# Optimization experiments

Hardware: AMD Instinct MI355X
Metric: run time of the kernel (lower is better)

## Reference

```python
import jax, jax.numpy as jnp
import numpy as np

B, S, D, CH = 1024, 64, 256, 1024


def setup_inputs() -> dict:
    key = jax.random.key(0)
    ks = jax.random.split(key, 8)
    sc = 0.05
    return {
        "local_descs_t": jax.random.normal(ks[0], (B, S, D), jnp.float32),
        "local_descs_rot": jax.random.normal(ks[1], (B, S, D), jnp.float32),
        "W_scene": jax.random.normal(ks[2], (2 * D, 1), jnp.float32) * sc,
        "b_scene": jnp.zeros((1,), jnp.float32),
        "Wt_h": jax.random.normal(ks[3], (S, D, CH), jnp.float32) * sc,
        "bt_h": jnp.zeros((S, CH), jnp.float32),
        "Wt_o": jax.random.normal(ks[4], (S, CH, 3), jnp.float32) * sc,
        "bt_o": jnp.zeros((S, 3), jnp.float32),
        "Wr_h": jax.random.normal(ks[5], (S, D, CH), jnp.float32) * sc,
        "br_h": jnp.zeros((S, CH), jnp.float32),
        "Wr_o": jax.random.normal(ks[6], (S, CH, 4), jnp.float32) * sc,
        "br_o": jnp.zeros((S, 4), jnp.float32),
    }


def reference(local_descs_t, local_descs_rot, W_scene, b_scene,
              Wt_h, bt_h, Wt_o, bt_o, Wr_h, br_h, Wr_o, br_o):
    # scene classifier: Linear(2D -> 1) on concat descriptors, log-softmax over scenes
    cat = jnp.concatenate((local_descs_t, local_descs_rot), axis=2)  # [B,S,2D]
    logits = jnp.einsum('bsd,do->bso', cat, W_scene)[..., 0] + b_scene[0]  # [B,S]
    scene_log_distr = jax.nn.log_softmax(logits, axis=1)
    max_idx = jnp.argmax(scene_log_distr, axis=1)  # [B] top-1 scene per sample

    b = jnp.arange(local_descs_t.shape[0])
    g_t = local_descs_t[b, max_idx]      # [B,D] one-hot gather of selected scene
    g_rot = local_descs_rot[b, max_idx]  # [B,D]

    h_t = jax.nn.gelu(jnp.einsum('bd,bdh->bh', g_t, Wt_h[max_idx]) + bt_h[max_idx],
                      approximate=False)
    x_t = jnp.einsum('bh,bho->bo', h_t, Wt_o[max_idx]) + bt_o[max_idx]  # [B,3]
    h_r = jax.nn.gelu(jnp.einsum('bd,bdh->bh', g_rot, Wr_h[max_idx]) + br_h[max_idx],
                      approximate=False)
    x_rot = jnp.einsum('bh,bho->bo', h_r, Wr_o[max_idx]) + br_o[max_idx]  # [B,4]

    expected_pose = jnp.concatenate((x_t, x_rot), axis=1)  # [B,7]
    return expected_pose, scene_log_distr
```

## Files before the change

kernel.cpp:

```cpp
#include <hip/hip_runtime.h>
#include <math.h>

#define BN 1024
#define SN 64
#define DN 256
#define CHN 1024
#define GRP 16

__device__ __forceinline__ float gelu_exact(float x) {
    return 0.5f * x * (1.0f + erff(x * 0.70710678118654752440f));
}

__global__ __launch_bounds__(256, 4) void k_scene(
    const float* __restrict__ dt, const float* __restrict__ dr,
    const float* __restrict__ Wsc, const float* __restrict__ bsc,
    const float* __restrict__ bt_o, const float* __restrict__ br_o,
    float* __restrict__ out_logd, float* __restrict__ pose,
    int* __restrict__ counts, int* __restrict__ lists)
{
    int b = blockIdx.x;
    int tid = threadIdx.x;
    int lane = tid & 63;
    int wave = tid >> 6;
    __shared__ float part[SN][65];
    __shared__ float logits[SN];

    float4 wt = *(const float4*)&Wsc[4 * lane];
    float4 wr = *(const float4*)&Wsc[DN + 4 * lane];
    const float* pt = dt + (size_t)b * SN * DN + 4 * lane;
    const float* pr = dr + (size_t)b * SN * DN + 4 * lane;
    float bias0 = bsc[0];

    float p[16];
    #pragma unroll 8
    for (int k = 0; k < 16; k++) {
        int s = wave * 16 + k;
        float4 t4 = *(const float4*)&pt[s * DN];
        float4 r4 = *(const float4*)&pr[s * DN];
        p[k] = t4.x * wt.x + t4.y * wt.y + t4.z * wt.z + t4.w * wt.w
             + r4.x * wr.x + r4.y * wr.y + r4.z * wr.z + r4.w * wr.w;
    }
    #pragma unroll
    for (int k = 0; k < 16; k++) part[wave * 16 + k][lane] = p[k];
    __syncthreads();

    {
        int s = tid >> 2, q = tid & 3;
        float sum = 0.f;
        #pragma unroll
        for (int j = 0; j < 16; j++) sum += part[s][q * 16 + j];
        sum += __shfl_xor(sum, 1);
        sum += __shfl_xor(sum, 2);
        if (q == 0) logits[s] = sum + bias0;
    }
    __syncthreads();

    if (wave == 0) {
        float l = logits[lane];
        float m = l; int idx = lane;
        #pragma unroll
        for (int off = 32; off >= 1; off >>= 1) {
            float om = __shfl_xor(m, off);
            int oidx = __shfl_xor(idx, off);
            if (om > m || (om == m && oidx < idx)) { m = om; idx = oidx; }
        }
        float e = expf(l - m);
        float ssum = e;
        #pragma unroll
        for (int off = 32; off >= 1; off >>= 1) ssum += __shfl_xor(ssum, off);
        float logZ = m + logf(ssum);
        out_logd[b * SN + lane] = l - logZ;
        if (lane == 0) {
            int pos = atomicAdd(&counts[idx], 1);
            lists[idx * BN + pos] = b;
        }
        if (lane < 7)
            pose[b * 7 + lane] = (lane < 3) ? bt_o[idx * 3 + lane]
                                            : br_o[idx * 4 + (lane - 3)];
    }
}

__global__ __launch_bounds__(256, 4) void k_expert(
    const float* __restrict__ dt, const float* __restrict__ dr,
    const float* __restrict__ Wt_h, const float* __restrict__ bt_h, const float* __restrict__ Wt_o,
    const float* __restrict__ Wr_h, const float* __restrict__ br_h, const float* __restrict__ Wr_o,
    const int* __restrict__ counts, const int* __restrict__ lists,
    float* __restrict__ pose)
{
    __shared__ float g[GRP][DN];
    __shared__ int pref[SN + 1];
    __shared__ int bl[GRP];
    int tid = threadIdx.x;
    int lane = tid & 63;
    int wave = tid >> 6;

    if (wave == 0) {
        int c = counts[lane];
        int ng = (c + 15) >> 4;
        #pragma unroll
        for (int off = 1; off < 64; off <<= 1) {
            int v = __shfl_up(ng, off);
            if (lane >= off) ng += v;
        }
        pref[lane + 1] = ng;
        if (lane == 0) pref[0] = 0;
    }
    __syncthreads();

    int q = blockIdx.x;
    if (q >= pref[SN] * 8) return;

    int s = 0;
    while (pref[s + 1] * 8 <= q) s++;
    int r = q - pref[s] * 8;
    int grp = r >> 3;
    int z = (r >> 2) & 1;
    int c4 = r & 3;

    int cnt = counts[s];
    int base = grp * GRP;
    int n = min(GRP, cnt - base);

    const float* Wh; const float* bh; const float* Wo; const float* descs; int no, ob;
    if (z == 0) {
        Wh = Wt_h + (size_t)s * DN * CHN; bh = bt_h + s * CHN;
        Wo = Wt_o + (size_t)s * CHN * 3;  descs = dt; no = 3; ob = 0;
    } else {
        Wh = Wr_h + (size_t)s * DN * CHN; bh = br_h + s * CHN;
        Wo = Wr_o + (size_t)s * CHN * 4;  descs = dr; no = 4; ob = 3;
    }

    #pragma unroll 4
    for (int i = 0; i < GRP; i++) {
        int bi = 0; float v = 0.f;
        if (i < n) {
            bi = lists[s * BN + base + i];
            v = descs[(size_t)bi * SN * DN + s * DN + tid];
        }
        g[i][tid] = v;
        if (tid == 0) bl[i] = bi;
    }
    __syncthreads();

    int h0 = c4 * 256 + tid;
    const float* wp = Wh + h0;
    float acc[GRP];
    #pragma unroll
    for (int i = 0; i < GRP; i++) acc[i] = 0.f;

    for (int db = 0; db < DN; db += 8) {
        float w[8];
        #pragma unroll
        for (int rr = 0; rr < 8; rr++) w[rr] = wp[(size_t)(db + rr) * CHN];
        #pragma unroll
        for (int i = 0; i < GRP; i++) {
            float4 ga = *(const float4*)&g[i][db];
            float4 gb = *(const float4*)&g[i][db + 4];
            acc[i] += ga.x * w[0] + ga.y * w[1] + ga.z * w[2] + ga.w * w[3]
                    + gb.x * w[4] + gb.y * w[5] + gb.z * w[6] + gb.w * w[7];
        }
    }

    float hb = bh[h0];
    float wo[4];
    #pragma unroll
    for (int o = 0; o < 4; o++) wo[o] = (o < no) ? Wo[h0 * no + o] : 0.f;

    #pragma unroll
    for (int i = 0; i < GRP; i++) {
        if (i < n) {
            float hv = gelu_exact(acc[i] + hb);
            #pragma unroll
            for (int o = 0; o < 4; o++) {
                if (o < no) {
                    float p = hv * wo[o];
                    #pragma unroll
                    for (int off = 32; off >= 1; off >>= 1) p += __shfl_down(p, off);
                    if (lane == 0) atomicAdd(&pose[bl[i] * 7 + ob + o], p);
                }
            }
        }
    }
}

extern "C" void kernel_launch(void* const* d_in, const int* in_sizes, int n_in,
                              void* d_out, int out_size, void* d_ws, size_t ws_size,
                              hipStream_t stream) {
    const float* dt    = (const float*)d_in[0];
    const float* dr    = (const float*)d_in[1];
    const float* Wsc   = (const float*)d_in[2];
    const float* bsc   = (const float*)d_in[3];
    const float* Wt_h  = (const float*)d_in[4];
    const float* bt_h  = (const float*)d_in[5];
    const float* Wt_o  = (const float*)d_in[6];
    const float* bt_o  = (const float*)d_in[7];
    const float* Wr_h  = (const float*)d_in[8];
    const float* br_h  = (const float*)d_in[9];
    const float* Wr_o  = (const float*)d_in[10];
    const float* br_o  = (const float*)d_in[11];

    float* pose = (float*)d_out;
    float* logd = (float*)d_out + BN * 7;

    int* counts  = (int*)((char*)d_ws + 4096);
    int* lists   = (int*)((char*)d_ws + 8192);

    hipMemsetAsync(counts, 0, SN * sizeof(int), stream);

    k_scene<<<BN, 256, 0, stream>>>(dt, dr, Wsc, bsc, bt_o, br_o,
                                    logd, pose, counts, lists);
    k_expert<<<1024, 256, 0, stream>>>(
        dt, dr, Wt_h, bt_h, Wt_o, Wr_h, br_h, Wr_o, counts, lists, pose);
}
```

Measured before the change: 303.3 us.

## Double expert group size, split reduction dim across half-blocks, double-buffer weight loads

Expert groups grow from 16 to 32 samples, so each expert hidden-weight column is streamed from memory half as often per sample. To keep per-thread work bounded, each block covers 128 hidden columns and splits the D reduction between its two 128-thread halves, combining partial sums through shared memory. Weight loads are double-buffered to overlap with the FMAs, and descriptor gathers use float4. The cost is more accumulator registers, an extra shared-memory combine with barriers, and idle upper-half threads during the GELU and output epilogue.

```diff
diff --git a/kernel.cpp b/kernel.cpp
--- a/kernel.cpp
+++ b/kernel.cpp
@@ -5,7 +5,7 @@
 #define SN 64
 #define DN 256
 #define CHN 1024
-#define GRP 16
+#define GRP 32
 
 __device__ __forceinline__ float gelu_exact(float x) {
     return 0.5f * x * (1.0f + erff(x * 0.70710678118654752440f));
@@ -92,11 +92,11 @@
     __shared__ int bl[GRP];
     int tid = threadIdx.x;
     int lane = tid & 63;
-    int wave = tid >> 6;
-
-    if (wave == 0) {
+    int wavei = tid >> 6;
+
+    if (wavei == 0) {
         int c = counts[lane];
-        int ng = (c + 15) >> 4;
+        int ng = (c + GRP - 1) >> 5;
         #pragma unroll
         for (int off = 1; off < 64; off <<= 1) {
             int v = __shfl_up(ng, off);
@@ -108,18 +108,22 @@
     __syncthreads();
 
     int q = blockIdx.x;
-    if (q >= pref[SN] * 8) return;
+    if (q >= pref[SN] * 16) return;
 
     int s = 0;
-    while (pref[s + 1] * 8 <= q) s++;
-    int r = q - pref[s] * 8;
-    int grp = r >> 3;
-    int z = (r >> 2) & 1;
-    int c4 = r & 3;
+    while (pref[s + 1] * 16 <= q) s++;
+    int r = q - pref[s] * 16;
+    int grp = r >> 4;
+    int z = (r >> 3) & 1;
+    int chunk = r & 7;
 
     int cnt = counts[s];
     int base = grp * GRP;
     int n = min(GRP, cnt - base);
+
+    int col = tid & 127;
+    int dh = tid >> 7;
+    int h0 = (chunk << 7) + col;
 
     const float* Wh; const float* bh; const float* Wo; const float* descs; int no, ob;
     if (z == 0) {
@@ -130,36 +134,64 @@
         Wo = Wr_o + (size_t)s * CHN * 4;  descs = dr; no = 4; ob = 3;
     }
 
-    #pragma unroll 4
-    for (int i = 0; i < GRP; i++) {
-        int bi = 0; float v = 0.f;
+    #pragma unroll 2
+    for (int ii = 0; ii < 8; ii++) {
+        int i = ii * 4 + wavei;
+        int bi = 0;
+        float4 v = make_float4(0.f, 0.f, 0.f, 0.f);
         if (i < n) {
             bi = lists[s * BN + base + i];
-            v = descs[(size_t)bi * SN * DN + s * DN + tid];
-        }
-        g[i][tid] = v;
-        if (tid == 0) bl[i] = bi;
-    }
-    __syncthreads();
-
-    int h0 = c4 * 256 + tid;
-    const float* wp = Wh + h0;
+            v = *(const float4*)&descs[(size_t)bi * SN * DN + s * DN + 4 * lane];
+        }
+        *(float4*)&g[i][4 * lane] = v;
+        if (lane == 0) bl[i] = bi;
+    }
+    __syncthreads();
+
+    int d0 = dh << 7;
+    const float* wp = Wh + (size_t)d0 * CHN + h0;
+
     float acc[GRP];
     #pragma unroll
     for (int i = 0; i < GRP; i++) acc[i] = 0.f;
 
-    for (int db = 0; db < DN; db += 8) {
-        float w[8];
-        #pragma unroll
-        for (int rr = 0; rr < 8; rr++) w[rr] = wp[(size_t)(db + rr) * CHN];
+    float wa[8], wb[8];
+    #pragma unroll
+    for (int rr = 0; rr < 8; rr++) wa[rr] = wp[(size_t)rr * CHN];
+
+    auto compute = [&](const float (&w)[8], int db) {
         #pragma unroll
         for (int i = 0; i < GRP; i++) {
-            float4 ga = *(const float4*)&g[i][db];
-            float4 gb = *(const float4*)&g[i][db + 4];
+            float4 ga = *(const float4*)&g[i][d0 + db];
+            float4 gb = *(const float4*)&g[i][d0 + db + 4];
             acc[i] += ga.x * w[0] + ga.y * w[1] + ga.z * w[2] + ga.w * w[3]
                     + gb.x * w[4] + gb.y * w[5] + gb.z * w[6] + gb.w * w[7];
         }
-    }
+    };
+
+    for (int db = 0; db < 112; db += 16) {
+        #pragma unroll
+        for (int rr = 0; rr < 8; rr++) wb[rr] = wp[(size_t)(db + 8 + rr) * CHN];
+        compute(wa, db);
+        #pragma unroll
+        for (int rr = 0; rr < 8; rr++) wa[rr] = wp[(size_t)(db + 16 + rr) * CHN];
+        compute(wb, db + 8);
+    }
+    #pragma unroll
+    for (int rr = 0; rr < 8; rr++) wb[rr] = wp[(size_t)(120 + rr) * CHN];
+    compute(wa, 112);
+    compute(wb, 120);
+
+    __syncthreads();
+    float* comb = &g[0][0];
+    if (dh == 1) {
+        #pragma unroll
+        for (int i = 0; i < GRP; i++) comb[i * 128 + col] = acc[i];
+    }
+    __syncthreads();
+    if (dh == 1) return;
+    #pragma unroll
+    for (int i = 0; i < GRP; i++) acc[i] += comb[i * 128 + col];
 
     float hb = bh[h0];
     float wo[4];
@@ -209,6 +241,6 @@
 
     k_scene<<<BN, 256, 0, stream>>>(dt, dr, Wsc, bsc, bt_o, br_o,
                                     logd, pose, counts, lists);
-    k_expert<<<1024, 256, 0, stream>>>(
+    k_expert<<<1536, 256, 0, stream>>>(
         dt, dr, Wt_h, bt_h, Wt_o, Wr_h, br_h, Wr_o, counts, lists, pose);
 }
```

Measured after the change: 317.5 us. +4.7%, slower.

## Split expert hidden matmul across waves over D with float4 weights and LDS reduction

Applied to the files above, without the earlier changes.

Each wave of the expert kernel now covers a 64-wide slice of D, and each lane computes 4 adjacent hidden units using float4 weight loads. The four waves' partial sums are then combined through two rounds of shared-memory reduction. Only wave 0 runs the GELU and output projection, folding the 4 hidden units per lane before the shuffle reduction, so each block issues fewer shuffles and atomics. The grid shrinks from 1024 to 992 blocks, which could drop groups if the scene distribution is very uneven. The extra barriers and a second 16 KB shared buffer may also lower occupancy.

```diff
diff --git a/kernel.cpp b/kernel.cpp
--- a/kernel.cpp
+++ b/kernel.cpp
@@ -88,15 +88,16 @@
     float* __restrict__ pose)
 {
     __shared__ float g[GRP][DN];
+    __shared__ float comb[GRP][DN];
     __shared__ int pref[SN + 1];
     __shared__ int bl[GRP];
     int tid = threadIdx.x;
     int lane = tid & 63;
-    int wave = tid >> 6;
-
-    if (wave == 0) {
+    int wv = tid >> 6;
+
+    if (tid < 64) {
         int c = counts[lane];
-        int ng = (c + 15) >> 4;
+        int ng = (c + GRP - 1) >> 4;
         #pragma unroll
         for (int off = 1; off < 64; off <<= 1) {
             int v = __shfl_up(ng, off);
@@ -115,7 +116,7 @@
     int r = q - pref[s] * 8;
     int grp = r >> 3;
     int z = (r >> 2) & 1;
-    int c4 = r & 3;
+    int chunk = r & 3;
 
     int cnt = counts[s];
     int base = grp * GRP;
@@ -142,38 +143,86 @@
     }
     __syncthreads();
 
-    int h0 = c4 * 256 + tid;
-    const float* wp = Wh + h0;
-    float acc[GRP];
-    #pragma unroll
-    for (int i = 0; i < GRP; i++) acc[i] = 0.f;
-
-    for (int db = 0; db < DN; db += 8) {
-        float w[8];
-        #pragma unroll
-        for (int rr = 0; rr < 8; rr++) w[rr] = wp[(size_t)(db + rr) * CHN];
+    int d0 = wv << 6;
+    int h0 = (chunk << 8) + lane * 4;
+    const float* wp = Wh + (size_t)d0 * CHN + h0;
+
+    float4 acc[GRP];
+    #pragma unroll
+    for (int i = 0; i < GRP; i++) acc[i] = make_float4(0.f, 0.f, 0.f, 0.f);
+
+    #pragma unroll 2
+    for (int st = 0; st < 16; st++) {
+        int db = st * 4;
+        float4 w0 = *(const float4*)&wp[(size_t)(db + 0) * CHN];
+        float4 w1 = *(const float4*)&wp[(size_t)(db + 1) * CHN];
+        float4 w2 = *(const float4*)&wp[(size_t)(db + 2) * CHN];
+        float4 w3 = *(const float4*)&wp[(size_t)(db + 3) * CHN];
         #pragma unroll
         for (int i = 0; i < GRP; i++) {
-            float4 ga = *(const float4*)&g[i][db];
-            float4 gb = *(const float4*)&g[i][db + 4];
-            acc[i] += ga.x * w[0] + ga.y * w[1] + ga.z * w[2] + ga.w * w[3]
-                    + gb.x * w[4] + gb.y * w[5] + gb.z * w[6] + gb.w * w[7];
-        }
-    }
-
-    float hb = bh[h0];
-    float wo[4];
-    #pragma unroll
-    for (int o = 0; o < 4; o++) wo[o] = (o < no) ? Wo[h0 * no + o] : 0.f;
+            float4 gv = *(const float4*)&g[i][d0 + db];
+            acc[i].x += gv.x * w0.x + gv.y * w1.x + gv.z * w2.x + gv.w * w3.x;
+            acc[i].y += gv.x * w0.y + gv.y * w1.y + gv.z * w2.y + gv.w * w3.y;
+            acc[i].z += gv.x * w0.z + gv.y * w1.z + gv.z * w2.z + gv.w * w3.z;
+            acc[i].w += gv.x * w0.w + gv.y * w1.w + gv.z * w2.w + gv.w * w3.w;
+        }
+    }
+
+    __syncthreads();
+    if (wv == 2) {
+        #pragma unroll
+        for (int i = 0; i < GRP; i++) *(float4*)&g[i][lane * 4] = acc[i];
+    } else if (wv == 3) {
+        #pragma unroll
+        for (int i = 0; i < GRP; i++) *(float4*)&comb[i][lane * 4] = acc[i];
+    }
+    __syncthreads();
+    if (wv == 0) {
+        #pragma unroll
+        for (int i = 0; i < GRP; i++) {
+            float4 v = *(const float4*)&g[i][lane * 4];
+            acc[i].x += v.x; acc[i].y += v.y; acc[i].z += v.z; acc[i].w += v.w;
+        }
+    } else if (wv == 1) {
+        #pragma unroll
+        for (int i = 0; i < GRP; i++) {
+            float4 v = *(const float4*)&comb[i][lane * 4];
+            acc[i].x += v.x; acc[i].y += v.y; acc[i].z += v.z; acc[i].w += v.w;
+        }
+    }
+    __syncthreads();
+    if (wv == 1) {
+        #pragma unroll
+        for (int i = 0; i < GRP; i++) *(float4*)&g[i][lane * 4] = acc[i];
+    }
+    __syncthreads();
+    if (wv != 0) return;
+    #pragma unroll
+    for (int i = 0; i < GRP; i++) {
+        float4 v = *(const float4*)&g[i][lane * 4];
+        acc[i].x += v.x; acc[i].y += v.y; acc[i].z += v.z; acc[i].w += v.w;
+    }
+
+    float4 hb4 = *(const float4*)&bh[h0];
+    float wo[4][4];
+    #pragma unroll
+    for (int c = 0; c < 4; c++)
+        #pragma unroll
+        for (int o = 0; o < 4; o++)
+            wo[o][c] = (o < no) ? Wo[(size_t)(h0 + c) * no + o] : 0.f;
 
     #pragma unroll
     for (int i = 0; i < GRP; i++) {
         if (i < n) {
-            float hv = gelu_exact(acc[i] + hb);
+            float hx = gelu_exact(acc[i].x + hb4.x);
+            float hy = gelu_exact(acc[i].y + hb4.y);
+            float hz = gelu_exact(acc[i].z + hb4.z);
+            float hw = gelu_exact(acc[i].w + hb4.w);
             #pragma unroll
             for (int o = 0; o < 4; o++) {
                 if (o < no) {
-                    float p = hv * wo[o];
+                    float p = hx * wo[o][0] + hy * wo[o][1]
+                            + hz * wo[o][2] + hw * wo[o][3];
                     #pragma unroll
                     for (int off = 32; off >= 1; off >>= 1) p += __shfl_down(p, off);
                     if (lane == 0) atomicAdd(&pose[bl[i] * 7 + ob + o], p);
@@ -209,6 +258,6 @@
 
     k_scene<<<BN, 256, 0, stream>>>(dt, dr, Wsc, bsc, bt_o, br_o,
                                     logd, pose, counts, lists);
-    k_expert<<<1024, 256, 0, stream>>>(
+    k_expert<<<992, 256, 0, stream>>>(
         dt, dr, Wt_h, bt_h, Wt_o, Wr_h, br_h, Wr_o, counts, lists, pose);
 }
```

New measurement: 299.6 us. No clear change (-1.2%).

## Double-buffer expert weight tiles into LDS via direct global-to-LDS loads

Applied to the files above, without the earlier changes.

The expert kernel now streams 16-row weight tiles straight from global memory into LDS with global_load_lds. It double-buffers them so the next tile loads while the current one is being multiplied. The per-thread work is remapped so each wave handles 4 samples and each lane 4 adjacent hidden columns, with float4 LDS reads and a combined output reduction. The goal is to replace scattered, strided per-thread scalar weight loads with coalesced async staging and more register reuse. In exchange it adds 32KB of LDS per block, which can lower occupancy, and it relies on barriers to cover completion of the async loads. The grid is also trimmed to the tight upper bound on group count.

```diff
diff --git a/kernel.cpp b/kernel.cpp
--- a/kernel.cpp
+++ b/kernel.cpp
@@ -7,8 +7,16 @@
 #define CHN 1024
 #define GRP 16
 
+#define LDS_AS __attribute__((address_space(3)))
+#define GLB_AS __attribute__((address_space(1)))
+
 __device__ __forceinline__ float gelu_exact(float x) {
     return 0.5f * x * (1.0f + erff(x * 0.70710678118654752440f));
+}
+
+__device__ __forceinline__ void stage_row(const float* gsrc_lane, float* lds_row) {
+    __builtin_amdgcn_global_load_lds((const GLB_AS void*)gsrc_lane,
+                                     (LDS_AS void*)lds_row, 16, 0, 0);
 }
 
 __global__ __launch_bounds__(256, 4) void k_scene(
@@ -88,15 +96,16 @@
     float* __restrict__ pose)
 {
     __shared__ float g[GRP][DN];
+    __shared__ float wbuf[2][16][DN];
     __shared__ int pref[SN + 1];
     __shared__ int bl[GRP];
     int tid = threadIdx.x;
     int lane = tid & 63;
-    int wave = tid >> 6;
-
-    if (wave == 0) {
+    int wv = tid >> 6;
+
+    if (tid < 64) {
         int c = counts[lane];
-        int ng = (c + 15) >> 4;
+        int ng = (c + GRP - 1) >> 4;
         #pragma unroll
         for (int off = 1; off < 64; off <<= 1) {
             int v = __shfl_up(ng, off);
@@ -115,7 +124,7 @@
     int r = q - pref[s] * 8;
     int grp = r >> 3;
     int z = (r >> 2) & 1;
-    int c4 = r & 3;
+    int chunk = r & 3;
 
     int cnt = counts[s];
     int base = grp * GRP;
@@ -130,6 +139,14 @@
         Wo = Wr_o + (size_t)s * CHN * 4;  descs = dr; no = 4; ob = 3;
     }
 
+    const float* wcol = Wh + (chunk << 8) + lane * 4;
+
+    #pragma unroll
+    for (int k = 0; k < 4; k++) {
+        int rr = wv * 4 + k;
+        stage_row(wcol + (size_t)rr * CHN, &wbuf[0][rr][0]);
+    }
+
     #pragma unroll 4
     for (int i = 0; i < GRP; i++) {
         int bi = 0; float v = 0.f;
@@ -142,41 +159,67 @@
     }
     __syncthreads();
 
-    int h0 = c4 * 256 + tid;
-    const float* wp = Wh + h0;
-    float acc[GRP];
-    #pragma unroll
-    for (int i = 0; i < GRP; i++) acc[i] = 0.f;
-
-    for (int db = 0; db < DN; db += 8) {
-        float w[8];
-        #pragma unroll
-        for (int rr = 0; rr < 8; rr++) w[rr] = wp[(size_t)(db + rr) * CHN];
-        #pragma unroll
-        for (int i = 0; i < GRP; i++) {
-            float4 ga = *(const float4*)&g[i][db];
-            float4 gb = *(const float4*)&g[i][db + 4];
-            acc[i] += ga.x * w[0] + ga.y * w[1] + ga.z * w[2] + ga.w * w[3]
-                    + gb.x * w[4] + gb.y * w[5] + gb.z * w[6] + gb.w * w[7];
-        }
-    }
-
-    float hb = bh[h0];
-    float wo[4];
-    #pragma unroll
-    for (int o = 0; o < 4; o++) wo[o] = (o < no) ? Wo[h0 * no + o] : 0.f;
-
-    #pragma unroll
-    for (int i = 0; i < GRP; i++) {
-        if (i < n) {
-            float hv = gelu_exact(acc[i] + hb);
+    int lane4 = lane * 4;
+    int i0 = wv * 4;
+
+    float4 acc[4];
+    #pragma unroll
+    for (int ii = 0; ii < 4; ii++) acc[ii] = make_float4(0.f, 0.f, 0.f, 0.f);
+
+    #pragma unroll 2
+    for (int t = 0; t < 16; t++) {
+        int cur = t & 1;
+        if (t < 15) {
+            #pragma unroll
+            for (int k = 0; k < 4; k++) {
+                int rr = wv * 4 + k;
+                stage_row(wcol + (size_t)((t + 1) * 16 + rr) * CHN,
+                          &wbuf[cur ^ 1][rr][0]);
+            }
+        }
+        #pragma unroll
+        for (int rg = 0; rg < 4; rg++) {
+            float4 w0 = *(const float4*)&wbuf[cur][rg * 4 + 0][lane4];
+            float4 w1 = *(const float4*)&wbuf[cur][rg * 4 + 1][lane4];
+            float4 w2 = *(const float4*)&wbuf[cur][rg * 4 + 2][lane4];
+            float4 w3 = *(const float4*)&wbuf[cur][rg * 4 + 3][lane4];
+            #pragma unroll
+            for (int ii = 0; ii < 4; ii++) {
+                float4 gv = *(const float4*)&g[i0 + ii][t * 16 + rg * 4];
+                acc[ii].x += gv.x * w0.x + gv.y * w1.x + gv.z * w2.x + gv.w * w3.x;
+                acc[ii].y += gv.x * w0.y + gv.y * w1.y + gv.z * w2.y + gv.w * w3.y;
+                acc[ii].z += gv.x * w0.z + gv.y * w1.z + gv.z * w2.z + gv.w * w3.z;
+                acc[ii].w += gv.x * w0.w + gv.y * w1.w + gv.z * w2.w + gv.w * w3.w;
+            }
+        }
+        __syncthreads();
+    }
+
+    int h0 = (chunk << 8) + lane4;
+    float4 hb4 = *(const float4*)&bh[h0];
+    float wo[4][4];
+    #pragma unroll
+    for (int c = 0; c < 4; c++)
+        #pragma unroll
+        for (int o = 0; o < 4; o++)
+            wo[o][c] = (o < no) ? Wo[(size_t)(h0 + c) * no + o] : 0.f;
+
+    #pragma unroll
+    for (int ii = 0; ii < 4; ii++) {
+        int si = i0 + ii;
+        if (si < n) {
+            float hx = gelu_exact(acc[ii].x + hb4.x);
+            float hy = gelu_exact(acc[ii].y + hb4.y);
+            float hz = gelu_exact(acc[ii].z + hb4.z);
+            float hw = gelu_exact(acc[ii].w + hb4.w);
             #pragma unroll
             for (int o = 0; o < 4; o++) {
                 if (o < no) {
-                    float p = hv * wo[o];
+                    float p = hx * wo[o][0] + hy * wo[o][1]
+                            + hz * wo[o][2] + hw * wo[o][3];
                     #pragma unroll
                     for (int off = 32; off >= 1; off >>= 1) p += __shfl_down(p, off);
-                    if (lane == 0) atomicAdd(&pose[bl[i] * 7 + ob + o], p);
+                    if (lane == 0) atomicAdd(&pose[bl[si] * 7 + ob + o], p);
                 }
             }
         }
@@ -209,6 +252,6 @@
 
     k_scene<<<BN, 256, 0, stream>>>(dt, dr, Wsc, bsc, bt_o, br_o,
                                     logd, pose, counts, lists);
-    k_expert<<<1024, 256, 0, stream>>>(
+    k_expert<<<992, 256, 0, stream>>>(
         dt, dr, Wt_h, bt_h, Wt_o, Wr_h, br_h, Wr_o, counts, lists, pose);
 }
```

Measured after the change: 290.8 us. -4.1%, faster.
